# Performance work log

Hardware: AMD Instinct MI355X
Metric: run time of the kernel (lower is better)

Reference implementation:

```python
import jax, jax.numpy as jnp
import numpy as np

N = 131072      # total nodes
B = 512         # number of graphs
F_DIM = 512     # in_channels
H = F_DIM // 2  # score_net hidden
RATIO = 0.5
MARGIN = 0.5
TOPK_LOSS_WEIGHT = 0.2


def setup_inputs() -> dict:
    key = jax.random.key(0)
    k1, k2, k3 = jax.random.split(key, 3)
    x = jax.random.normal(k1, (N, F_DIM), dtype=jnp.float32)
    # sorted segment ids: equal-sized graphs of N // B nodes
    batch = (jnp.arange(N) // (N // B)).astype(jnp.int32)
    W1 = jax.random.normal(k2, (F_DIM, H), dtype=jnp.float32) / np.sqrt(F_DIM).astype(np.float32)
    b1 = jnp.zeros((H,), dtype=jnp.float32)
    W2 = jax.random.normal(k3, (H, 1), dtype=jnp.float32) / np.sqrt(H).astype(np.float32)
    b2 = jnp.zeros((1,), dtype=jnp.float32)
    return {"x": x, "batch": batch, "W1": W1, "b1": b1, "W2": W2, "b2": b2}


def reference(x, batch, W1, b1, W2, b2):
    # scores = score_net(x).squeeze(-1)   [N]
    scores = (jax.nn.relu(x @ W1 + b1) @ W2 + b2)[:, 0]

    # per-graph node counts and k = max(1, int(ratio * n_i))
    counts = jax.ops.segment_sum(jnp.ones((N,), dtype=scores.dtype), batch, num_segments=B)
    k = jnp.maximum(1, jnp.floor(RATIO * counts).astype(jnp.int32))  # [B]

    # segmented top-k via lexsort: sort by (batch asc, score desc)
    order = jnp.lexsort((-scores, batch))          # [N] permutation
    b_sorted = batch[order]
    starts = jnp.cumsum(counts) - counts           # exclusive-cumsum segment starts
    rank = jnp.arange(N, dtype=counts.dtype) - starts[b_sorted]  # rank within graph (0 = highest score)
    sel_sorted = rank < k[b_sorted].astype(counts.dtype)
    selected_mask = jnp.zeros((N,), dtype=bool).at[order].set(sel_sorted)

    # global_add_pool over selected nodes
    m = selected_mask.astype(x.dtype)
    x_pooled = jax.ops.segment_sum(x * m[:, None], batch, num_segments=B)  # [B, F]

    # margin regularization loss per graph
    sel_cnt = jax.ops.segment_sum(m, batch, num_segments=B)
    sel_sum = jax.ops.segment_sum(scores * m, batch, num_segments=B)
    tot_sum = jax.ops.segment_sum(scores, batch, num_segments=B)
    uns_cnt = counts - sel_cnt
    sel_mean = sel_sum / jnp.maximum(sel_cnt, 1.0)
    uns_mean = (tot_sum - sel_sum) / jnp.maximum(uns_cnt, 1.0)
    per_graph = jnp.where(uns_cnt > 0, jax.nn.relu(MARGIN - (sel_mean - uns_mean)), 0.0)
    topk_loss = per_graph.sum() / B * TOPK_LOSS_WEIGHT

    return x_pooled, topk_loss, selected_mask
```

## Files before the change

### kernel.cpp

```cpp
#include <hip/hip_runtime.h>

#define BGRAPHS 512
#define FDIM    512
#define HDIM    256
#define NPG     256
#define KSEL    128
#define STAGES  32
#define BSTAGE_SHORTS 8192
#define A_ROW   24
#define A_PLANE (128 * A_ROW)

typedef __attribute__((ext_vector_type(8)))  _Float16 f16x8;
typedef __attribute__((ext_vector_type(8)))  short    s16x8;
typedef __attribute__((ext_vector_type(16))) float    f32x16;

__device__ __forceinline__ unsigned short f16_rne(float f, float* back) {
    _Float16 h = (_Float16)f;
    *back = (float)h;
    union { _Float16 h; unsigned short s; } cv; cv.h = h;
    return cv.s;
}

__global__ __launch_bounds__(256)
void split_w1_kernel(const float* __restrict__ W1, unsigned short* __restrict__ wsB)
{
    const int uid  = blockIdx.x * 256 + threadIdx.x;
    const int lane = uid & 63;
    int t = uid >> 6;
    const int nt = t & 7;  t >>= 3;
    const int p  = t & 1;  t >>= 1;
    const int s  = t;
    const int n  = nt * 32 + (lane & 31);
    const int k0 = s * 16 + (lane >> 5) * 8;

    s16x8 v;
    #pragma unroll
    for (int j = 0; j < 8; ++j) {
        float w = W1[(size_t)(k0 + j) * HDIM + n] * 1024.0f;
        float f1, f2;
        unsigned short h1 = f16_rne(w, &f1);
        unsigned short h2 = f16_rne(w - f1, &f2);
        v[j] = (short)(p ? h2 : h1);
    }
    *(s16x8*)(wsB + (size_t)uid * 8) = v;
}

__global__ __launch_bounds__(512, 4)
void gemm_kernel(const float* __restrict__ x,
                 const unsigned short* __restrict__ wsB,
                 const float* __restrict__ b1, const float* __restrict__ W2,
                 const float* __restrict__ b2,
                 float* __restrict__ scores_out)
{
    __shared__ __attribute__((aligned(16))) unsigned char smem[57344];

    const int bid  = blockIdx.x;
    const int g    = bid >> 1;
    const int rh   = bid & 1;
    const int tid  = threadIdx.x;
    const int lane = tid & 63;
    const int wv   = tid >> 6;
    const int wy   = wv & 1;
    const int wx   = wv >> 1;
    const int l31  = lane & 31;
    const int lh   = lane >> 5;

    const int arow  = tid >> 2;
    const int achk  = tid & 3;
    const float* aptr = x + ((size_t)(g * NPG + rh * 128 + arow)) * FDIM + achk * 4;

    f32x16 acc[2][2];
    #pragma unroll
    for (int a = 0; a < 2; ++a)
        #pragma unroll
        for (int b = 0; b < 2; ++b)
            #pragma unroll
            for (int rr = 0; rr < 16; ++rr) acc[a][b][rr] = 0.f;

    float4 aA, aB;

#define GLL_B(S1) do {                                                          \
    const unsigned short* _src = wsB + (size_t)(S1) * BSTAGE_SHORTS;            \
    unsigned short* _dst = (unsigned short*)smem + ((S1) & 1) * BSTAGE_SHORTS;  \
    _Pragma("unroll")                                                           \
    for (int _i = 0; _i < 2; ++_i) {                                            \
        const int _u = _i * 512 + tid;                                          \
        __builtin_amdgcn_global_load_lds(                                       \
            (const __attribute__((address_space(1))) unsigned int*)(_src + (size_t)_u * 8), \
            (__attribute__((address_space(3))) unsigned int*)(_dst + _u * 8),   \
            16, 0, 0);                                                          \
    } } while (0)

#define LOAD_PF(P,S2) do { P = *(const float4*)(aptr + (S2) * 16); } while (0)

#define CONVERT_A(P,BUF) do {                                                   \
    float _f[4] = {P.x, P.y, P.z, P.w};                                         \
    unsigned short _H[4], _M[4];                                                \
    _Pragma("unroll")                                                           \
    for (int _j = 0; _j < 4; ++_j) {                                            \
        float _b1v, _b2v;                                                       \
        float _xs = _f[_j] * 64.0f;                            \
        _H[_j] = f16_rne(_xs, &_b1v);                                           \
        _M[_j] = f16_rne(_xs - _b1v, &_b2v);                                    \
        (void)_b2v;                                                             \
    }                                                                           \
    unsigned short* _pl = (unsigned short*)(smem + 32768 + (BUF) * 12288)       \
                          + arow * A_ROW + achk * 4;                            \
    uint2 _uH, _uM;                                                             \
    _uH.x = (unsigned)_H[0] | ((unsigned)_H[1] << 16);                          \
    _uH.y = (unsigned)_H[2] | ((unsigned)_H[3] << 16);                          \
    _uM.x = (unsigned)_M[0] | ((unsigned)_M[1] << 16);                          \
    _uM.y = (unsigned)_M[2] | ((unsigned)_M[3] << 16);                          \
    *(uint2*)_pl = _uH;                                                         \
    *(uint2*)(_pl + A_PLANE) = _uM;                                             \
    } while (0)

#define COMPUTE(BUF) do {                                                       \
    const f16x8* _bfp = (const f16x8*)(smem + (BUF) * (BSTAGE_SHORTS * 2));     \
    const unsigned short* _aB = (const unsigned short*)(smem + 32768 + (BUF) * 12288); \
    const int _a0 = (wy * 64 + l31) * A_ROW + lh * 8;                           \
    f16x8 A0h = *(const f16x8*)(_aB + _a0);                                     \
    f16x8 A0m = *(const f16x8*)(_aB + A_PLANE + _a0);                           \
    f16x8 A1h = *(const f16x8*)(_aB + _a0 + 32 * A_ROW);                        \
    f16x8 A1m = *(const f16x8*)(_aB + A_PLANE + _a0 + 32 * A_ROW);              \
    const int _nn = wx * 2;                                                     \
    f16x8 Bh0 = _bfp[(0 * 8 + _nn + 0) * 64 + lane];                            \
    f16x8 Bh1 = _bfp[(0 * 8 + _nn + 1) * 64 + lane];                            \
    f16x8 Bm0 = _bfp[(1 * 8 + _nn + 0) * 64 + lane];                            \
    f16x8 Bm1 = _bfp[(1 * 8 + _nn + 1) * 64 + lane];                            \
    acc[0][0] = __builtin_amdgcn_mfma_f32_32x32x16_f16(A0h, Bh0, acc[0][0], 0, 0, 0); \
    acc[0][1] = __builtin_amdgcn_mfma_f32_32x32x16_f16(A0h, Bh1, acc[0][1], 0, 0, 0); \
    acc[1][0] = __builtin_amdgcn_mfma_f32_32x32x16_f16(A1h, Bh0, acc[1][0], 0, 0, 0); \
    acc[1][1] = __builtin_amdgcn_mfma_f32_32x32x16_f16(A1h, Bh1, acc[1][1], 0, 0, 0); \
    acc[0][0] = __builtin_amdgcn_mfma_f32_32x32x16_f16(A0m, Bh0, acc[0][0], 0, 0, 0); \
    acc[0][1] = __builtin_amdgcn_mfma_f32_32x32x16_f16(A0m, Bh1, acc[0][1], 0, 0, 0); \
    acc[1][0] = __builtin_amdgcn_mfma_f32_32x32x16_f16(A1m, Bh0, acc[1][0], 0, 0, 0); \
    acc[1][1] = __builtin_amdgcn_mfma_f32_32x32x16_f16(A1m, Bh1, acc[1][1], 0, 0, 0); \
    acc[0][0] = __builtin_amdgcn_mfma_f32_32x32x16_f16(A0h, Bm0, acc[0][0], 0, 0, 0); \
    acc[0][1] = __builtin_amdgcn_mfma_f32_32x32x16_f16(A0h, Bm1, acc[0][1], 0, 0, 0); \
    acc[1][0] = __builtin_amdgcn_mfma_f32_32x32x16_f16(A1h, Bm0, acc[1][0], 0, 0, 0); \
    acc[1][1] = __builtin_amdgcn_mfma_f32_32x32x16_f16(A1h, Bm1, acc[1][1], 0, 0, 0); \
    } while (0)

    LOAD_PF(aA, 0);
    GLL_B(0);
    CONVERT_A(aA, 0);
    LOAD_PF(aA, 1);
    __syncthreads();

    for (int s = 0; s < STAGES; s += 2) {
        if (s < STAGES - 1) GLL_B(s + 1);
        if (s < STAGES - 2) LOAD_PF(aB, s + 2);
        COMPUTE(0);
        if (s < STAGES - 1) CONVERT_A(aA, 1);
        __syncthreads();

        if (s + 1 < STAGES - 1) GLL_B(s + 2);
        if (s + 1 < STAGES - 2) LOAD_PF(aA, s + 3);
        COMPUTE(1);
        if (s + 1 < STAGES - 1) CONVERT_A(aB, 0);
        __syncthreads();
    }

    float* scr = (float*)smem;

    float bb[2], ww[2];
    #pragma unroll
    for (int nt = 0; nt < 2; ++nt) {
        const int cc = wx * 64 + nt * 32 + l31;
        bb[nt] = b1[cc];
        ww[nt] = W2[cc];
    }
    const float unscale = 1.0f / 65536.0f;
    #pragma unroll
    for (int mt = 0; mt < 2; ++mt) {
        float pr[16];
        #pragma unroll
        for (int rr = 0; rr < 16; ++rr) pr[rr] = 0.f;
        #pragma unroll
        for (int nt = 0; nt < 2; ++nt)
            #pragma unroll
            for (int rr = 0; rr < 16; ++rr) {
                float h = fmaf(acc[mt][nt][rr], unscale, bb[nt]);
                h = h > 0.f ? h : 0.f;
                pr[rr] = fmaf(h, ww[nt], pr[rr]);
            }
        #pragma unroll
        for (int mask = 1; mask <= 16; mask <<= 1)
            #pragma unroll
            for (int rr = 0; rr < 16; ++rr)
                pr[rr] += __shfl_xor(pr[rr], mask);
        if (l31 == 0) {
            #pragma unroll
            for (int rr = 0; rr < 16; ++rr) {
                const int row = wy * 64 + mt * 32 + (rr & 3) + 8 * (rr >> 2) + 4 * lh;
                scr[wx * 128 + row] = pr[rr];
            }
        }
    }
    __syncthreads();

    if (tid < 128) {
        const float s = b2[0] + scr[tid] + scr[128 + tid] + scr[256 + tid] + scr[384 + tid];
        scores_out[g * NPG + rh * 128 + tid] = s;
    }

#undef GLL_B
#undef LOAD_PF
#undef CONVERT_A
#undef COMPUTE
}

__global__ __launch_bounds__(512)
void select_pool_kernel(const float* __restrict__ x,
                        float* __restrict__ scores_mask,
                        float* __restrict__ pooled,
                        float* __restrict__ loss_per_g)
{
    __shared__ float sv[NPG];
    __shared__ int   selr[KSEL];
    __shared__ float redT[NPG];
    __shared__ float redS[NPG];

    const int g   = blockIdx.x;
    const int tid = threadIdx.x;

    float sc = 0.f;
    if (tid < NPG) {
        sc = scores_mask[g * NPG + tid];
        sv[tid] = sc;
    }
    __syncthreads();

    if (tid < NPG) {
        int rank = 0;
        for (int j = 0; j < NPG; ++j) {
            const float sj = sv[j];
            rank += (sj > sc || (sj == sc && j < tid)) ? 1 : 0;
        }
        const bool sel = rank < KSEL;
        scores_mask[g * NPG + tid] = sel ? 1.0f : 0.0f;
        if (sel) selr[rank] = tid;
        redT[tid] = sc;
        redS[tid] = sel ? sc : 0.f;
    }
    __syncthreads();

    for (int off = 128; off > 0; off >>= 1) {
        if (tid < off) { redT[tid] += redT[tid + off]; redS[tid] += redS[tid + off]; }
        __syncthreads();
    }
    if (tid == 0) {
        const float tot = redT[0], ssum = redS[0];
        const float sel_mean = ssum * (1.0f / KSEL);
        const float uns_mean = (tot - ssum) * (1.0f / (NPG - KSEL));
        const float v = 0.5f - (sel_mean - uns_mean);
        loss_per_g[g] = v > 0.f ? v : 0.f;
    }

    const int col = tid;
    const float* __restrict__ xg = x + (size_t)g * NPG * FDIM;
    float a0 = 0.f, a1 = 0.f, a2 = 0.f, a3 = 0.f;
    float a4 = 0.f, a5 = 0.f, a6 = 0.f, a7 = 0.f;
    #pragma unroll 2
    for (int n = 0; n < KSEL; n += 8) {
        a0 += xg[(size_t)selr[n + 0] * FDIM + col];
        a1 += xg[(size_t)selr[n + 1] * FDIM + col];
        a2 += xg[(size_t)selr[n + 2] * FDIM + col];
        a3 += xg[(size_t)selr[n + 3] * FDIM + col];
        a4 += xg[(size_t)selr[n + 4] * FDIM + col];
        a5 += xg[(size_t)selr[n + 5] * FDIM + col];
        a6 += xg[(size_t)selr[n + 6] * FDIM + col];
        a7 += xg[(size_t)selr[n + 7] * FDIM + col];
    }
    pooled[g * FDIM + col] = ((a0 + a1) + (a2 + a3)) + ((a4 + a5) + (a6 + a7));
}

__global__ __launch_bounds__(256)
void loss_kernel(const float* __restrict__ loss_per_g, float* __restrict__ out_loss)
{
    __shared__ float red[256];
    const int t = threadIdx.x;
    red[t] = loss_per_g[t] + loss_per_g[t + 256];
    __syncthreads();
    for (int off = 128; off > 0; off >>= 1) {
        if (t < off) red[t] += red[t + off];
        __syncthreads();
    }
    if (t == 0) out_loss[0] = red[0] * (0.2f / BGRAPHS);
}

extern "C" void kernel_launch(void* const* d_in, const int* in_sizes, int n_in,
                              void* d_out, int out_size, void* d_ws, size_t ws_size,
                              hipStream_t stream)
{
    const float* x  = (const float*)d_in[0];
    const float* W1 = (const float*)d_in[2];
    const float* b1 = (const float*)d_in[3];
    const float* W2 = (const float*)d_in[4];
    const float* b2 = (const float*)d_in[5];

    float* out    = (float*)d_out;
    float* pooled = out;
    float* loss   = out + BGRAPHS * FDIM;
    float* mask   = loss + 1;

    float* loss_g       = (float*)d_ws;
    unsigned short* wsB = (unsigned short*)((char*)d_ws + 4096);

    split_w1_kernel<<<128, 256, 0, stream>>>(W1, wsB);
    gemm_kernel<<<2 * BGRAPHS, 512, 0, stream>>>(x, wsB, b1, W2, b2, mask);
    select_pool_kernel<<<BGRAPHS, 512, 0, stream>>>(x, mask, pooled, loss_g);
    loss_kernel<<<1, 256, 0, stream>>>(loss_g, loss);
}
```

Baseline: 426.2 us.

## Triple-buffer B tiles in LDS with partial vmcnt waits and MFMA priority

```diff
diff --git a/kernel.cpp b/kernel.cpp
--- a/kernel.cpp
+++ b/kernel.cpp
@@ -7,6 +7,7 @@
 #define KSEL    128
 #define STAGES  32
 #define BSTAGE_SHORTS 8192
+#define BSTG    16384
 #define A_ROW   24
 #define A_PLANE (128 * A_ROW)
 
@@ -52,7 +53,7 @@
                  const float* __restrict__ b2,
                  float* __restrict__ scores_out)
 {
-    __shared__ __attribute__((aligned(16))) unsigned char smem[57344];
+    __shared__ __attribute__((aligned(16))) unsigned char smem[73728];
 
     const int bid  = blockIdx.x;
     const int g    = bid >> 1;
@@ -77,11 +78,11 @@
             #pragma unroll
             for (int rr = 0; rr < 16; ++rr) acc[a][b][rr] = 0.f;
 
-    float4 aA, aB;
-
-#define GLL_B(S1) do {                                                          \
+    float4 pfA, pfB;
+
+#define GLL_B(OFF, S1) do {                                                     \
     const unsigned short* _src = wsB + (size_t)(S1) * BSTAGE_SHORTS;            \
-    unsigned short* _dst = (unsigned short*)smem + ((S1) & 1) * BSTAGE_SHORTS;  \
+    unsigned short* _dst = (unsigned short*)(smem + (OFF));                     \
     _Pragma("unroll")                                                           \
     for (int _i = 0; _i < 2; ++_i) {                                            \
         const int _u = _i * 512 + tid;                                          \
@@ -104,7 +105,7 @@
         _M[_j] = f16_rne(_xs - _b1v, &_b2v);                                    \
         (void)_b2v;                                                             \
     }                                                                           \
-    unsigned short* _pl = (unsigned short*)(smem + 32768 + (BUF) * 12288)       \
+    unsigned short* _pl = (unsigned short*)(smem + 49152 + (BUF) * 12288)       \
                           + arow * A_ROW + achk * 4;                            \
     uint2 _uH, _uM;                                                             \
     _uH.x = (unsigned)_H[0] | ((unsigned)_H[1] << 16);                          \
@@ -115,9 +116,9 @@
     *(uint2*)(_pl + A_PLANE) = _uM;                                             \
     } while (0)
 
-#define COMPUTE(BUF) do {                                                       \
-    const f16x8* _bfp = (const f16x8*)(smem + (BUF) * (BSTAGE_SHORTS * 2));     \
-    const unsigned short* _aB = (const unsigned short*)(smem + 32768 + (BUF) * 12288); \
+#define COMPUTE(OFFB, ABUF) do {                                                \
+    const f16x8* _bfp = (const f16x8*)(smem + (OFFB));                          \
+    const unsigned short* _aB = (const unsigned short*)(smem + 49152 + (ABUF) * 12288); \
     const int _a0 = (wy * 64 + l31) * A_ROW + lh * 8;                           \
     f16x8 A0h = *(const f16x8*)(_aB + _a0);                                     \
     f16x8 A0m = *(const f16x8*)(_aB + A_PLANE + _a0);                           \
@@ -128,6 +129,7 @@
     f16x8 Bh1 = _bfp[(0 * 8 + _nn + 1) * 64 + lane];                            \
     f16x8 Bm0 = _bfp[(1 * 8 + _nn + 0) * 64 + lane];                            \
     f16x8 Bm1 = _bfp[(1 * 8 + _nn + 1) * 64 + lane];                            \
+    __builtin_amdgcn_s_setprio(1);                                              \
     acc[0][0] = __builtin_amdgcn_mfma_f32_32x32x16_f16(A0h, Bh0, acc[0][0], 0, 0, 0); \
     acc[0][1] = __builtin_amdgcn_mfma_f32_32x32x16_f16(A0h, Bh1, acc[0][1], 0, 0, 0); \
     acc[1][0] = __builtin_amdgcn_mfma_f32_32x32x16_f16(A1h, Bh0, acc[1][0], 0, 0, 0); \
@@ -140,27 +142,42 @@
     acc[0][1] = __builtin_amdgcn_mfma_f32_32x32x16_f16(A0h, Bm1, acc[0][1], 0, 0, 0); \
     acc[1][0] = __builtin_amdgcn_mfma_f32_32x32x16_f16(A1h, Bm0, acc[1][0], 0, 0, 0); \
     acc[1][1] = __builtin_amdgcn_mfma_f32_32x32x16_f16(A1h, Bm1, acc[1][1], 0, 0, 0); \
+    __builtin_amdgcn_s_setprio(0);                                              \
     } while (0)
 
-    LOAD_PF(aA, 0);
-    GLL_B(0);
-    CONVERT_A(aA, 0);
-    LOAD_PF(aA, 1);
-    __syncthreads();
-
-    for (int s = 0; s < STAGES; s += 2) {
-        if (s < STAGES - 1) GLL_B(s + 1);
-        if (s < STAGES - 2) LOAD_PF(aB, s + 2);
-        COMPUTE(0);
-        if (s < STAGES - 1) CONVERT_A(aA, 1);
-        __syncthreads();
-
-        if (s + 1 < STAGES - 1) GLL_B(s + 2);
-        if (s + 1 < STAGES - 2) LOAD_PF(aA, s + 3);
-        COMPUTE(1);
-        if (s + 1 < STAGES - 1) CONVERT_A(aB, 0);
-        __syncthreads();
-    }
+#define SYNC3 do {                                                              \
+    asm volatile("s_waitcnt vmcnt(3) lgkmcnt(0)" ::: "memory");                 \
+    __builtin_amdgcn_s_barrier();                                               \
+    __builtin_amdgcn_sched_barrier(0); } while (0)
+#define SYNC0 do {                                                              \
+    asm volatile("s_waitcnt vmcnt(0) lgkmcnt(0)" ::: "memory");                 \
+    __builtin_amdgcn_s_barrier();                                               \
+    __builtin_amdgcn_sched_barrier(0); } while (0)
+
+    LOAD_PF(pfA, 0);  GLL_B(0, 0);
+    LOAD_PF(pfB, 1);  GLL_B(BSTG, 1);
+    CONVERT_A(pfA, 0);
+    SYNC3;
+
+    int o0 = 0, o1 = BSTG, o2 = 2 * BSTG;
+    for (int s = 0; s < 30; s += 2) {
+        LOAD_PF(pfA, s + 2);  GLL_B(o2, s + 2);
+        COMPUTE(o0, 0);
+        CONVERT_A(pfB, 1);
+        SYNC3;
+
+        LOAD_PF(pfB, s + 3);  GLL_B(o0, s + 3);
+        COMPUTE(o1, 1);
+        CONVERT_A(pfA, 0);
+        SYNC3;
+
+        const int t = o0; o0 = o2; o2 = o1; o1 = t;
+    }
+
+    COMPUTE(o0, 0);
+    CONVERT_A(pfB, 1);
+    SYNC0;
+    COMPUTE(o1, 1);
 
     float* scr = (float*)smem;
 
@@ -209,6 +226,8 @@
 #undef LOAD_PF
 #undef CONVERT_A
 #undef COMPUTE
+#undef SYNC3
+#undef SYNC0
 }
 
 __global__ __launch_bounds__(512)
```

Measured after the change: 424.4 us. No clear change (-0.4%).
